# Optimization experiments

Measured on AMD Instinct MI355X. Metric: run time of the kernel, lower is better.

## Reference

```python
import jax, jax.numpy as jnp
import numpy as np

B, S, E, H, FF = 4, 2048, 512, 8, 2048
DH = E // H
EPS = 1e-6


def setup_inputs() -> dict:
    key = jax.random.key(0)
    ks = jax.random.split(key, 16)
    sc = lambda fan_in: 1.0 / np.sqrt(fan_in)
    inp = {
        "x": jax.random.normal(ks[0], (B, S, E), dtype=jnp.float32),
        "src_mask": jnp.ones((B, 1, 1, S), dtype=jnp.int32),
        # attention projections, stored [in, out]
        "wq": jax.random.uniform(ks[1], (E, E), minval=-sc(E), maxval=sc(E)),
        "bq": jnp.zeros((E,), jnp.float32),
        "wk": jax.random.uniform(ks[2], (E, E), minval=-sc(E), maxval=sc(E)),
        "bk": jnp.zeros((E,), jnp.float32),
        "wv": jax.random.uniform(ks[3], (E, E), minval=-sc(E), maxval=sc(E)),
        "bv": jnp.zeros((E,), jnp.float32),
        "wo": jax.random.uniform(ks[4], (E, E), minval=-sc(E), maxval=sc(E)),
        "bo": jnp.zeros((E,), jnp.float32),
        # feed-forward
        "w1": jax.random.uniform(ks[5], (E, FF), minval=-sc(E), maxval=sc(E)),
        "b1": jnp.zeros((FF,), jnp.float32),
        "w2": jax.random.uniform(ks[6], (FF, E), minval=-sc(FF), maxval=sc(FF)),
        "b2": jnp.zeros((E,), jnp.float32),
        # addNormLayer scalar params (alpha init 1, bias init 0)
        "alpha1": jnp.ones((1,), jnp.float32),
        "beta1": jnp.zeros((1,), jnp.float32),
        "alpha2": jnp.ones((1,), jnp.float32),
        "beta2": jnp.zeros((1,), jnp.float32),
    }
    return inp


def _norm(x, alpha, beta):
    # matches torch: mean + unbiased std (ddof=1), eps added to std
    mean = jnp.mean(x, axis=-1, keepdims=True)
    std = jnp.std(x, axis=-1, keepdims=True, ddof=1)
    return alpha * (x - mean) / (std + EPS) + beta


def reference(x, src_mask, wq, bq, wk, bk, wv, bv, wo, bo,
              w1, b1, w2, b2, alpha1, beta1, alpha2, beta2):
    # --- residual 1: pre-norm self-attention ---
    n = _norm(x, alpha1, beta1)  # [B,S,E]
    q = (n @ wq + bq).reshape(B, S, H, DH).transpose(0, 2, 1, 3)  # [B,H,S,DH]
    k = (n @ wk + bk).reshape(B, S, H, DH).transpose(0, 2, 1, 3)
    v = (n @ wv + bv).reshape(B, S, H, DH).transpose(0, 2, 1, 3)
    scores = jnp.einsum('bhqd,bhkd->bhqk', q, k) / np.sqrt(DH)  # [B,H,S,S]
    scores = jnp.where(src_mask == 0, -1e9, scores)
    attn = jax.nn.softmax(scores, axis=-1)
    ctx = jnp.einsum('bhqk,bhkd->bhqd', attn, v)  # [B,H,S,DH]
    ctx = ctx.transpose(0, 2, 1, 3).reshape(B, S, E)
    x = x + (ctx @ wo + bo)
    # --- residual 2: pre-norm FFN ---
    n2 = _norm(x, alpha2, beta2)
    ff = jax.nn.relu(n2 @ w1 + b1) @ w2 + b2
    return x + ff
```

## Files before the change

kernel.cpp:

```cpp
#include <hip/hip_runtime.h>
#include <type_traits>

typedef __bf16 bfrag __attribute__((ext_vector_type(8)));
typedef float f32x4 __attribute__((ext_vector_type(4)));
typedef float f32x16 __attribute__((ext_vector_type(16)));
typedef unsigned short us8 __attribute__((ext_vector_type(8)));
typedef unsigned short us4 __attribute__((ext_vector_type(4)));
typedef unsigned int u32x2 __attribute__((ext_vector_type(2)));
typedef unsigned int u32x4 __attribute__((ext_vector_type(4)));

__device__ __forceinline__ float bf2f(unsigned short s) {
  unsigned u = ((unsigned)s) << 16;
  float f;
  __builtin_memcpy(&f, &u, 4);
  return f;
}
__device__ __forceinline__ unsigned short f2bf(float f) {
  unsigned u;
  __builtin_memcpy(&u, &f, 4);
  u += 0x7fffu + ((u >> 16) & 1u);
  return (unsigned short)(u >> 16);
}
__device__ __forceinline__ float rdf(const void* p, size_t i, int isf) {
  return isf ? ((const float*)p)[i] : bf2f(((const unsigned short*)p)[i]);
}
__device__ __forceinline__ void gld16(const unsigned short* g, unsigned short* l) {
  __builtin_amdgcn_global_load_lds(
      (const __attribute__((address_space(1))) unsigned int*)g,
      (__attribute__((address_space(3))) unsigned int*)l, 16, 0, 0);
}
__device__ __forceinline__ unsigned cvtpk_bf16(float a, float b) {
  unsigned d;
  asm("v_cvt_pk_bf16_f32 %0, %1, %2" : "=v"(d) : "v"(a), "v"(b));
  return d;
}

template <int XMODE>
__device__ void norm_unit(const void* xin, const void* alpha, const void* beta,
                          unsigned short* out, int isf, int u) {
  constexpr int E = 512;
  int xf = XMODE ? 1 : isf;
  int tid = threadIdx.x;
  int wave = tid >> 6, lane = tid & 63;
  size_t tok = (size_t)u * 4 + wave;
  float v[8];
  if (xf) {
    const float* xp = (const float*)xin + tok * E + lane * 8;
    float4 a0 = *(const float4*)xp;
    float4 a1 = *(const float4*)(xp + 4);
    v[0] = a0.x; v[1] = a0.y; v[2] = a0.z; v[3] = a0.w;
    v[4] = a1.x; v[5] = a1.y; v[6] = a1.z; v[7] = a1.w;
  } else {
    us8 uu = *(const us8*)((const unsigned short*)xin + tok * E + lane * 8);
#pragma unroll
    for (int j = 0; j < 8; j++) v[j] = bf2f(uu[j]);
  }
  float s = 0.f, sq = 0.f;
#pragma unroll
  for (int j = 0; j < 8; j++) { s += v[j]; sq += v[j] * v[j]; }
#pragma unroll
  for (int off = 1; off < 64; off <<= 1) {
    s += __shfl_xor(s, off, 64);
    sq += __shfl_xor(sq, off, 64);
  }
  float mean = s * (1.0f / 512.0f);
  float var = fmaxf((sq - 512.0f * mean * mean) * (1.0f / 511.0f), 0.0f);
  float inv = rdf(alpha, 0, isf) / (sqrtf(var) + 1e-6f);
  float be = rdf(beta, 0, isf);
  us8 ov;
#pragma unroll
  for (int j = 0; j < 8; j++) ov[j] = f2bf((v[j] - mean) * inv + be);
  *(us8*)(out + tok * E + lane * 8) = ov;
}

__global__ __launch_bounds__(256) void setup_k(
    const unsigned short* __restrict__ x16,
    const void* wq, const void* wk, const void* wv, const void* wo,
    const void* w1, const void* w2,
    unsigned short* wqkvT, unsigned short* woT,
    unsigned short* w1T, unsigned short* w2T,
    const void* bq, const void* bk, const void* bv, const void* bo,
    const void* b1, const void* b2, float* __restrict__ bcat,
    const void* alpha1, const void* beta1, unsigned short* __restrict__ n1,
    int* __restrict__ flag) {
  __shared__ unsigned short tile[32][33];
  __shared__ int s_cnt;
  int tid = threadIdx.x;
  int bid = blockIdx.x;
  if (tid == 0) s_cnt = 0;
  __syncthreads();
  {
    int c = 0;
    for (int i = tid; i < 4096; i += 256) {
      unsigned short s = x16[2 * i];
      int e = (s >> 7) & 0xFF;
      if (e > 0xC2 || (e != 0 && e < 0x3D)) c++;
    }
    atomicAdd(&s_cnt, c);
  }
  __syncthreads();
  const int isf = (s_cnt > 256) ? 1 : 0;
  if (bid == 0 && tid == 0) flag[0] = isf;

  if (bid >= 3090) {
    norm_unit<0>(x16, alpha1, beta1, n1, isf, bid - 3090);
    return;
  }
  if (bid >= 3072) {
    int i = (bid - 3072) * 256 + tid;
    if (i < 4608) {
      float v;
      if (i < 512) v = rdf(bq, i, isf);
      else if (i < 1024) v = rdf(bk, i - 512, isf);
      else if (i < 1536) v = rdf(bv, i - 1024, isf);
      else if (i < 2048) v = rdf(bo, i - 1536, isf);
      else if (i < 4096) v = rdf(b1, i - 2048, isf);
      else v = rdf(b2, i - 4096, isf);
      bcat[i] = v;
    }
    return;
  }
  const void* W;
  unsigned short* Wt;
  int K, N, t;
  if (bid < 1024) {
    K = 512; N = 512; t = bid & 255;
    if (bid < 256) { W = wq; Wt = wqkvT; }
    else if (bid < 512) { W = wk; Wt = wqkvT + 262144; }
    else if (bid < 768) { W = wv; Wt = wqkvT + 524288; }
    else { W = wo; Wt = woT; }
  } else if (bid < 2048) {
    W = w1; Wt = w1T; K = 512; N = 2048; t = bid - 1024;
  } else {
    W = w2; Wt = w2T; K = 2048; N = 512; t = bid - 2048;
  }
  int nx = N >> 5;
  int n0 = (t % nx) * 32, k0 = (t / nx) * 32;
#pragma unroll
  for (int i = 0; i < 4; i++) {
    int e = tid + i * 256;
    int r = e >> 5, c = e & 31;
    tile[r][c] = f2bf(rdf(W, (size_t)(k0 + r) * N + n0 + c, isf));
  }
  __syncthreads();
#pragma unroll
  for (int i = 0; i < 4; i++) {
    int e = tid + i * 256;
    int r = e >> 5, c = e & 31;
    Wt[(size_t)(n0 + r) * K + k0 + c] = tile[c][r];
  }
}

__global__ __launch_bounds__(256) void norm2_k(
    const void* __restrict__ xin, const void* __restrict__ alpha,
    const void* __restrict__ beta, unsigned short* __restrict__ out,
    const int* __restrict__ flag) {
  norm_unit<1>(xin, alpha, beta, out, flag[0], blockIdx.x);
}

template <int TN, int RES, int OUTM, int RELU, int QSC, int VT>
__global__ __launch_bounds__(256, 3) void gemm2_k(
    const unsigned short* __restrict__ A,
    const unsigned short* __restrict__ Bt,
    const float* __restrict__ bias,
    const void* __restrict__ res,
    void* __restrict__ outp,
    unsigned short* __restrict__ vbt,
    int N, int K, const int* __restrict__ flag) {
  constexpr int MT = (TN == 128) ? 4 : 2;
  constexpr int BROWS = TN / 4;
  __shared__ alignas(16) unsigned short As[128 * 64];
  __shared__ alignas(16) unsigned short Bs[TN * 64];
  int isf = flag[0];
  int outf32 = (OUTM == 1) || (OUTM == 2 && isf);
  int tid = threadIdx.x;
  int wave = tid >> 6, lane = tid & 63;
  int quad = lane >> 4, l16 = lane & 15, l7 = l16 & 7;
  int wm = (TN == 128) ? (wave >> 1) : wave;
  int wn = (TN == 128) ? (wave & 1) : 0;

  int lin = (int)blockIdx.x + 64 * (int)blockIdx.y;
  int xcd = lin & 7, kk = lin >> 3;
  size_t m0 = (size_t)(xcd * 8 + (kk & 7)) * 128;
  size_t n0 = (size_t)(kk >> 3) * TN;

  int lrow = lane >> 3;
  int gcol = 8 * ((lane & 7) ^ lrow);

  const unsigned short* ag = A + (m0 + wave * 32 + lrow) * K + gcol;
  const unsigned short* bg = Bt + (n0 + wave * BROWS + lrow) * K + gcol;
  unsigned short* asl = &As[(wave * 32) * 64];
  unsigned short* bsl = &Bs[(wave * BROWS) * 64];

  f32x4 acc[MT][4];
#pragma unroll
  for (int i = 0; i < MT; i++)
#pragma unroll
    for (int j = 0; j < 4; j++) acc[i][j] = {0.f, 0.f, 0.f, 0.f};

  for (int k0 = 0; k0 < K; k0 += 64) {
    __syncthreads();
#pragma unroll
    for (int c = 0; c < 4; c++)
      gld16(ag + (size_t)(8 * c) * K + k0, asl + (8 * c) * 64);
#pragma unroll
    for (int c = 0; c < BROWS / 8; c++)
      gld16(bg + (size_t)(8 * c) * K + k0, bsl + (8 * c) * 64);
    __syncthreads();
#pragma unroll
    for (int ko = 0; ko < 2; ko++) {
      int slot = ((4 * ko + quad) ^ l7) * 8;
      bfrag af[MT], bf[4];
#pragma unroll
      for (int i = 0; i < MT; i++)
        af[i] = *(const bfrag*)&As[(wm * (MT * 16) + i * 16 + l16) * 64 + slot];
#pragma unroll
      for (int j = 0; j < 4; j++)
        bf[j] = *(const bfrag*)&Bs[(wn * 64 + j * 16 + l16) * 64 + slot];
#pragma unroll
      for (int i = 0; i < MT; i++)
#pragma unroll
        for (int j = 0; j < 4; j++)
          acc[i][j] = __builtin_amdgcn_mfma_f32_16x16x32_bf16(af[i], bf[j], acc[i][j], 0, 0, 0);
    }
  }
  if (VT && n0 >= 1024) {
    int bq = (int)(m0 >> 11);
    int sbase = (int)(m0 & 2047) + wm * (MT * 16) + quad * 4;
#pragma unroll
    for (int j = 0; j < 4; j++) {
      int n = (int)n0 + wn * 64 + j * 16 + l16;
      float bv = bias[n];
      int hh = (n - 1024) >> 6, d = (n - 1024) & 63;
      size_t row = ((size_t)(bq * 8 + hh) * 64 + d) * 2048;
#pragma unroll
      for (int i = 0; i < MT; i++) {
        us4 pk;
#pragma unroll
        for (int r = 0; r < 4; r++) pk[r] = f2bf(acc[i][j][r] + bv);
        *(us4*)&vbt[row + sbase + i * 16] = pk;
      }
    }
    return;
  }
#pragma unroll
  for (int j = 0; j < 4; j++) {
    size_t n = n0 + wn * 64 + j * 16 + l16;
    float bv = bias[n];
#pragma unroll
    for (int i = 0; i < MT; i++) {
#pragma unroll
      for (int r = 0; r < 4; r++) {
        size_t m = m0 + wm * (MT * 16) + i * 16 + quad * 4 + r;
        float vv = acc[i][j][r] + bv;
        if (QSC && n < 512) vv *= 0.18033688f;
        if (RELU) vv = fmaxf(vv, 0.0f);
        if (RES == 1) vv += rdf(res, m * N + n, isf);
        else if (RES == 2) vv += ((const float*)res)[m * N + n];
        if (outf32) ((float*)outp)[m * N + n] = vv;
        else ((unsigned short*)outp)[m * N + n] = f2bf(vv);
      }
    }
  }
}

__global__ __launch_bounds__(512) void attn_k(
    const unsigned short* __restrict__ qkb,
    const unsigned short* __restrict__ vbt,
    const int* __restrict__ mask,
    unsigned short* __restrict__ ctx) {
  constexpr int S = 2048;
  __shared__ alignas(16) unsigned short Kt[2][2][64 * 64];
  __shared__ alignas(16) unsigned short Vt[2][2][64 * 64];
  __shared__ alignas(16) float mskf[S];
  __shared__ float ml[2][256];
  __shared__ int s_all;
  int tid = threadIdx.x, wave = tid >> 6, lane = tid & 63;
  int kh = wave >> 2, wv = wave & 3;
  int l32 = lane & 31, hi = lane >> 5;

  int lin = blockIdx.x;
  int work = (lin & 7) * 32 + (lin >> 3);
  int bh = work >> 3;
  int q0 = (work & 7) * 256;
  int b = bh >> 3, h = bh & 7;
  size_t rowbase = (size_t)b * S;

  bfrag qf[2][4];
#pragma unroll
  for (int qg = 0; qg < 2; qg++) {
    const unsigned short* qp =
        qkb + (rowbase + q0 + wv * 64 + qg * 32 + l32) * 1536 + h * 64 + hi * 8;
#pragma unroll
    for (int ds = 0; ds < 4; ds++) qf[qg][ds] = *(const bfrag*)(qp + ds * 16);
  }

  int srow_l = lane >> 3;
  int sc = lane & 7;
  int swz = (sc ^ srow_l) * 8;
  const unsigned short* kgb = qkb + 512 + h * 64;
  const unsigned short* vgb = vbt + (size_t)bh * 64 * S;

  const unsigned short* kp[2];
  const unsigned short* vp[2];
#pragma unroll
  for (int i = 0; i < 2; i++) {
    int r = wv * 16 + i * 8 + srow_l;
    kp[i] = kgb + (rowbase + kh * 1024 + r) * 1536 + swz;
    vp[i] = vgb + (size_t)r * S + kh * 1024 + swz;
  }

  auto STAGE = [&](int buf) {
#pragma unroll
    for (int i = 0; i < 2; i++) {
      gld16(kp[i], &Kt[kh][buf][(wv * 16 + i * 8) * 64]);
      kp[i] += 64 * 1536;
      gld16(vp[i], &Vt[kh][buf][(wv * 16 + i * 8) * 64]);
      vp[i] += 64;
    }
  };

  f32x16 o[4];
#pragma unroll
  for (int i = 0; i < 4; i++)
#pragma unroll
    for (int j = 0; j < 16; j++) o[i][j] = 0.f;
  float l_i[2] = {0.f, 0.f};

  STAGE(0);
  if (tid == 0) s_all = 1;
  __syncthreads();
  {
    int ok = 1;
    for (int i = tid; i < S; i += 512) {
      int mv = mask[rowbase + i];
      ok &= (mv != 0);
      mskf[i] = mv ? 0.0f : -1e5f;
    }
    atomicAnd(&s_all, ok);
  }
  __syncthreads();
  int am = s_all;

  auto BODY = [&](auto amc) {
    constexpr bool AM = decltype(amc)::value;
    for (int it = 0; it < 16; it++) {
      int cur = it & 1;
      if (it + 1 < 16) STAGE(cur ^ 1);

#pragma unroll
      for (int qg = 0; qg < 2; qg++) {
#pragma unroll
        for (int t = 0; t < 2; t++) {
          f32x16 pacc;
          {
            int r = t * 32 + l32;
            f32x16 z = {};
#pragma unroll
            for (int ds = 0; ds < 4; ds++) {
              int phys = ((2 * ds + hi) ^ (l32 & 7)) * 8;
              bfrag kf = *(const bfrag*)&Kt[kh][cur][r * 64 + phys];
              pacc = __builtin_amdgcn_mfma_f32_32x32x16_bf16(
                  kf, qf[qg][ds], ds == 0 ? z : pacc, 0, 0, 0);
            }
          }
          unsigned pb[8];
#pragma unroll
          for (int g = 0; g < 4; g++) {
            float p0, p1, p2, p3;
            if constexpr (AM) {
              p0 = __builtin_amdgcn_exp2f(pacc[g * 4 + 0]);
              p1 = __builtin_amdgcn_exp2f(pacc[g * 4 + 1]);
              p2 = __builtin_amdgcn_exp2f(pacc[g * 4 + 2]);
              p3 = __builtin_amdgcn_exp2f(pacc[g * 4 + 3]);
            } else {
              float4 m4 =
                  *(const float4*)&mskf[kh * 1024 + it * 64 + t * 32 + g * 8 + hi * 4];
              p0 = __builtin_amdgcn_exp2f(pacc[g * 4 + 0] + m4.x);
              p1 = __builtin_amdgcn_exp2f(pacc[g * 4 + 1] + m4.y);
              p2 = __builtin_amdgcn_exp2f(pacc[g * 4 + 2] + m4.z);
              p3 = __builtin_amdgcn_exp2f(pacc[g * 4 + 3] + m4.w);
            }
            l_i[qg] += (p0 + p1) + (p2 + p3);
            pb[g * 2] = cvtpk_bf16(p0, p1);
            pb[g * 2 + 1] = cvtpk_bf16(p2, p3);
          }
#pragma unroll
          for (int e = 0; e < 2; e++) {
            u32x2 sA = __builtin_amdgcn_permlane32_swap(
                pb[4 * e + 0], pb[4 * e + 2], false, false);
            u32x2 sB = __builtin_amdgcn_permlane32_swap(
                pb[4 * e + 1], pb[4 * e + 3], false, false);
            u32x4 pw = {sA.x, sB.x, sA.y, sB.y};
            bfrag pf = __builtin_bit_cast(bfrag, pw);
            int ks = 2 * t + e;
#pragma unroll
            for (int dt = 0; dt < 2; dt++) {
              int r = dt * 32 + l32;
              int phys = ((2 * ks + hi) ^ (l32 & 7)) * 8;
              bfrag vf = *(const bfrag*)&Vt[kh][cur][r * 64 + phys];
              o[qg * 2 + dt] = __builtin_amdgcn_mfma_f32_32x32x16_bf16(
                  pf, vf, o[qg * 2 + dt], 0, 0, 0);
            }
          }
        }
      }
      __syncthreads();
    }
  };
  if (am) BODY(std::integral_constant<bool, true>{});
  else    BODY(std::integral_constant<bool, false>{});

#pragma unroll
  for (int qg = 0; qg < 2; qg++) {
    unsigned lu = __builtin_bit_cast(unsigned, l_i[qg]);
    u32x2 lr = __builtin_amdgcn_permlane32_swap(lu, lu, false, false);
    float l_tot = __builtin_bit_cast(float, lr.x) + __builtin_bit_cast(float, lr.y);
    if (lane < 32) ml[kh][wv * 64 + qg * 32 + l32] = l_tot;
  }
  float* mrgK = (float*)&Kt[0][0][0];
  float* mrgV = (float*)&Vt[0][0][0];
  if (kh == 1) {
#pragma unroll
    for (int qg = 0; qg < 2; qg++) {
#pragma unroll
      for (int reg = 0; reg < 16; reg++) {
        int ql = (reg & 3) + 8 * (reg >> 2) + 4 * hi;
        int qi = wv * 64 + qg * 32 + ql;
        mrgK[qi * 32 + l32] = o[qg * 2 + 0][reg];
        mrgV[qi * 32 + l32] = o[qg * 2 + 1][reg];
      }
    }
  }
  __syncthreads();
  if (kh == 0) {
#pragma unroll
    for (int qg = 0; qg < 2; qg++) {
#pragma unroll
      for (int reg = 0; reg < 16; reg++) {
        int ql = (reg & 3) + 8 * (reg >> 2) + 4 * hi;
        int qi = wv * 64 + qg * 32 + ql;
        float inv = 1.0f / fmaxf(ml[0][qi] + ml[1][qi], 1e-30f);
        size_t qrow = rowbase + q0 + qi;
        float v0 = (o[qg * 2 + 0][reg] + mrgK[qi * 32 + l32]) * inv;
        float v1 = (o[qg * 2 + 1][reg] + mrgV[qi * 32 + l32]) * inv;
        ctx[qrow * 512 + h * 64 + l32] = f2bf(v0);
        ctx[qrow * 512 + h * 64 + 32 + l32] = f2bf(v1);
      }
    }
  }
}

extern "C" void kernel_launch(void* const* d_in, const int* in_sizes, int n_in,
                              void* d_out, int out_size, void* d_ws, size_t ws_size,
                              hipStream_t stream) {
  const unsigned short* x = (const unsigned short*)d_in[0];
  const int* mask         = (const int*)d_in[1];
  const void* wq = d_in[2];  const void* bq = d_in[3];
  const void* wk = d_in[4];  const void* bk = d_in[5];
  const void* wv = d_in[6];  const void* bv = d_in[7];
  const void* wo = d_in[8];  const void* bo = d_in[9];
  const void* w1 = d_in[10]; const void* b1 = d_in[11];
  const void* w2 = d_in[12]; const void* b2 = d_in[13];
  const void* alpha1 = d_in[14]; const void* beta1 = d_in[15];
  const void* alpha2 = d_in[16]; const void* beta2 = d_in[17];

  char* ws = (char*)d_ws;
  int* flag            = (int*)(ws + 0);
  unsigned short* wqkvT= (unsigned short*)(ws + 65536);
  unsigned short* woT  = (unsigned short*)(ws + 1638400);
  unsigned short* w1T  = (unsigned short*)(ws + 2162688);
  unsigned short* w2T  = (unsigned short*)(ws + 4259840);
  float*          bcat = (float*)         (ws + 6356992);
  float*          x1   = (float*)         (ws + 6422528);
  unsigned short* n1   = (unsigned short*)(ws + 23199744);
  unsigned short* qkb  = (unsigned short*)(ws + 31588352);
  unsigned short* vbt  = (unsigned short*)(ws + 56754176);
  unsigned short* ff1  = qkb;

  dim3 blk(256);

  setup_k<<<5138, blk, 0, stream>>>(x, wq, wk, wv, wo, w1, w2,
                                    wqkvT, woT, w1T, w2T,
                                    bq, bk, bv, bo, b1, b2, bcat,
                                    alpha1, beta1, n1, flag);
  gemm2_k<128, 0, 0, 0, 1, 1><<<dim3(64, 12), blk, 0, stream>>>(n1, wqkvT, bcat, nullptr, qkb, vbt, 1536, 512, flag);
  attn_k<<<256, dim3(512), 0, stream>>>(qkb, vbt, mask, n1);
  gemm2_k<64, 1, 1, 0, 0, 0><<<dim3(64, 8), blk, 0, stream>>>(n1, woT, bcat + 1536, (const void*)x, x1, nullptr, 512, 512, flag);
  norm2_k<<<2048, blk, 0, stream>>>(x1, alpha2, beta2, n1, flag);
  gemm2_k<128, 0, 0, 1, 0, 0><<<dim3(64, 16), blk, 0, stream>>>(n1, w1T, bcat + 2048, nullptr, ff1, nullptr, 2048, 512, flag);
  gemm2_k<64, 2, 2, 0, 0, 0><<<dim3(64, 8), blk, 0, stream>>>(ff1, w2T, bcat + 4096, x1, d_out, nullptr, 512, 2048, flag);
}
```

Before: 267.3 us.

## Stage transposed V tile through shared memory and drop XCD-aware block swizzle

The V-transpose epilogue of the QKV GEMM now writes the tile into padded shared memory and then emits coalesced 16-byte stores per row of the transposed V buffer, replacing scattered 8-byte stores. This targets poorly coalesced global writes for the V^T output. The change also removes the XCD-aware block index remapping and uses plain blockIdx for tile coordinates, which may hurt L2 locality across chiplets. The VT variant's shared memory grows to hold the padded tile.

```diff
diff --git a/kernel.cpp b/kernel.cpp
--- a/kernel.cpp
+++ b/kernel.cpp
@@ -5,7 +5,6 @@
 typedef float f32x4 __attribute__((ext_vector_type(4)));
 typedef float f32x16 __attribute__((ext_vector_type(16)));
 typedef unsigned short us8 __attribute__((ext_vector_type(8)));
-typedef unsigned short us4 __attribute__((ext_vector_type(4)));
 typedef unsigned int u32x2 __attribute__((ext_vector_type(2)));
 typedef unsigned int u32x4 __attribute__((ext_vector_type(4)));
 
@@ -169,8 +168,10 @@
     int N, int K, const int* __restrict__ flag) {
   constexpr int MT = (TN == 128) ? 4 : 2;
   constexpr int BROWS = TN / 4;
-  __shared__ alignas(16) unsigned short As[128 * 64];
-  __shared__ alignas(16) unsigned short Bs[TN * 64];
+  constexpr int SM = VT ? (128 * 136) : (128 * 64 + TN * 64);
+  __shared__ alignas(16) unsigned short smem[SM];
+  unsigned short* As = smem;
+  unsigned short* Bs = smem + 128 * 64;
   int isf = flag[0];
   int outf32 = (OUTM == 1) || (OUTM == 2 && isf);
   int tid = threadIdx.x;
@@ -178,11 +179,8 @@
   int quad = lane >> 4, l16 = lane & 15, l7 = l16 & 7;
   int wm = (TN == 128) ? (wave >> 1) : wave;
   int wn = (TN == 128) ? (wave & 1) : 0;
-
-  int lin = (int)blockIdx.x + 64 * (int)blockIdx.y;
-  int xcd = lin & 7, kk = lin >> 3;
-  size_t m0 = (size_t)(xcd * 8 + (kk & 7)) * 128;
-  size_t n0 = (size_t)(kk >> 3) * TN;
+  size_t m0 = (size_t)blockIdx.x * 128;
+  size_t n0 = (size_t)blockIdx.y * TN;
 
   int lrow = lane >> 3;
   int gcol = 8 * ((lane & 7) ^ lrow);
@@ -225,21 +223,32 @@
     }
   }
   if (VT && n0 >= 1024) {
-    int bq = (int)(m0 >> 11);
-    int sbase = (int)(m0 & 2047) + wm * (MT * 16) + quad * 4;
+    __syncthreads();
 #pragma unroll
     for (int j = 0; j < 4; j++) {
-      int n = (int)n0 + wn * 64 + j * 16 + l16;
-      float bv = bias[n];
-      int hh = (n - 1024) >> 6, d = (n - 1024) & 63;
-      size_t row = ((size_t)(bq * 8 + hh) * 64 + d) * 2048;
+      int nl = wn * 64 + j * 16 + l16;
+      float bv = bias[n0 + nl];
 #pragma unroll
       for (int i = 0; i < MT; i++) {
-        us4 pk;
-#pragma unroll
-        for (int r = 0; r < 4; r++) pk[r] = f2bf(acc[i][j][r] + bv);
-        *(us4*)&vbt[row + sbase + i * 16] = pk;
+#pragma unroll
+        for (int r = 0; r < 4; r++) {
+          int ml = wm * (MT * 16) + i * 16 + quad * 4 + r;
+          smem[nl * 136 + ml] = f2bf(acc[i][j][r] + bv);
+        }
       }
+    }
+    __syncthreads();
+    int b_ = (int)(m0 >> 11);
+    int sbase = (int)(m0 & 2047);
+    int rel0 = (int)n0 - 1024;
+#pragma unroll
+    for (int it2 = 0; it2 < 8; it2++) {
+      int nl = (tid >> 2) + 64 * (it2 & 1);
+      int mc = (tid & 3) + 4 * (it2 >> 1);
+      int rel = rel0 + nl;
+      size_t row = ((size_t)(b_ * 8 + (rel >> 6)) * 64 + (rel & 63)) * 2048;
+      us8 v = *(const us8*)&smem[nl * 136 + mc * 8];
+      *(us8*)&vbt[row + sbase + mc * 8] = v;
     }
     return;
   }
```

Measured after the change: 266.2 us. About the same (-0.4%).
